# Optimization experiments

Hardware: AMD Instinct MI355X
Metric: run time of the kernel (lower is better)

Reference implementation:

```python
import jax, jax.numpy as jnp
import numpy as np

B, T, D, H = 2, 2048, 2048, 16
DH = D // H

def setup_inputs() -> dict:
    key = jax.random.key(0)
    k1, k2, k3 = jax.random.split(key, 3)
    x = jax.random.normal(k1, (B, T, D), dtype=jnp.float32)
    w_qkv = jax.random.normal(k2, (D, 3 * D), dtype=jnp.float32) * (1.0 / np.sqrt(D))
    w_o = jax.random.normal(k3, (D, D), dtype=jnp.float32) * (1.0 / np.sqrt(D))
    return {"x": x, "w_qkv": w_qkv, "w_o": w_o}

def reference(x, w_qkv, w_o):
    b, t, d = x.shape
    qkv = (x @ w_qkv).reshape(b, t, 3, H, DH)
    q, k, v = qkv[:, :, 0], qkv[:, :, 1], qkv[:, :, 2]  # [b,t,h,dh]
    scale = 1.0 / np.sqrt(DH).astype(np.float32)
    # scores: [b,h,t,t]
    scores = jnp.einsum('bqhd,bkhd->bhqk', q, k) * scale
    causal = jnp.tril(jnp.ones((t, t), dtype=bool))
    scores = jnp.where(causal[None, None], scores, -jnp.inf)
    attn = jax.nn.softmax(scores, axis=-1)
    out = jnp.einsum('bhqk,bkhd->bqhd', attn, v).reshape(b, t, d)
    return out @ w_o
```

## Files before the change

### kernel.cpp

```cpp
#include <hip/hip_runtime.h>
#include <hip/hip_bf16.h>

#define B_   2
#define T_   2048
#define D_   2048
#define H_   16
#define DH_  128
#define TD3_ 6144

typedef __attribute__((ext_vector_type(8))) short   short8;
typedef __attribute__((ext_vector_type(8))) unsigned short ushort8v;
typedef __attribute__((ext_vector_type(4))) float   f32x4;
typedef __attribute__((ext_vector_type(4))) float   f4v;
typedef __attribute__((ext_vector_type(4))) unsigned short u16x4;

static __device__ __forceinline__ unsigned short f2bf(float f) {
  unsigned int u = __builtin_bit_cast(unsigned int, f);
  u += 0x7FFFu + ((u >> 16) & 1u);
  return (unsigned short)(u >> 16);
}
static __device__ __forceinline__ float bf2f(unsigned short u) {
  return __builtin_bit_cast(float, (unsigned int)u << 16);
}

static __device__ __forceinline__ void gload_lds16(const unsigned short* g, unsigned short* l) {
  __builtin_amdgcn_global_load_lds((const __attribute__((address_space(1))) void*)g,
                                   (__attribute__((address_space(3))) void*)l, 16, 0, 0);
}

__global__ __launch_bounds__(256) void convert_f32_bf16(const float* __restrict__ X,
                                                        unsigned short* __restrict__ Y, int n4) {
  for (int i = blockIdx.x * blockDim.x + threadIdx.x; i < n4; i += gridDim.x * blockDim.x) {
    f4v v = ((const f4v*)X)[i];
    u16x4 o;
    o[0] = f2bf(v[0]); o[1] = f2bf(v[1]); o[2] = f2bf(v[2]); o[3] = f2bf(v[3]);
    ((u16x4*)Y)[i] = o;
  }
}

__global__ __launch_bounds__(256) void transpose_f32_bf16(const float* __restrict__ W,
                                                          unsigned short* __restrict__ WT,
                                                          int K, int N) {
  __shared__ float tile[32][33];
  int n0 = blockIdx.x * 32, k0 = blockIdx.y * 32;
  int tx = threadIdx.x & 31, ty = threadIdx.x >> 5;
#pragma unroll
  for (int r = 0; r < 4; r++)
    tile[ty + 8 * r][tx] = W[(size_t)(k0 + ty + 8 * r) * N + n0 + tx];
  __syncthreads();
#pragma unroll
  for (int r = 0; r < 4; r++)
    WT[(size_t)(n0 + ty + 8 * r) * K + k0 + tx] = f2bf(tile[tx][ty + 8 * r]);
}

__global__ __launch_bounds__(256) void vtr_kernel(const unsigned short* __restrict__ qkv,
                                                  unsigned short* __restrict__ vtg) {
  __shared__ unsigned short tile[64][68];
  const int t0 = blockIdx.x * 64;
  const int h = blockIdx.y >> 1, dh0 = (blockIdx.y & 1) * 64;
  const int b = blockIdx.z;
  const int tid = threadIdx.x;
  const unsigned short* src = qkv + (size_t)b * T_ * TD3_ + 2 * D_ + h * DH_ + dh0;
  {
    const int r = tid >> 3, cc = (tid & 7) * 8;
#pragma unroll
    for (int k = 0; k < 2; k++) {
      ushort8v v = *(const ushort8v*)(src + (size_t)(t0 + k * 32 + r) * TD3_ + cc);
      *(ushort8v*)&tile[k * 32 + r][cc] = v;
    }
  }
  __syncthreads();
  unsigned short* dst = vtg + ((size_t)(b * H_ + h) * DH_ + dh0) * T_ + t0;
  {
    const int d = tid >> 3, tc = (tid & 7) * 8;
#pragma unroll
    for (int k = 0; k < 2; k++) {
      ushort8v v;
#pragma unroll
      for (int j = 0; j < 8; j++) v[j] = tile[tc + j][k * 32 + d];
      *(ushort8v*)(dst + (size_t)(k * 32 + d) * T_ + tc) = v;
    }
  }
}

__global__ __launch_bounds__(512, 1) void gemm256(const unsigned short* __restrict__ A,
                                                  const unsigned short* __restrict__ BT,
                                                  unsigned short* __restrict__ C,
                                                  int M, int N, int K) {
  __shared__ unsigned short lA[2][2][128 * 64];
  __shared__ unsigned short lB[2][2][128 * 64];

  const int tid = threadIdx.x;
  const int bid = (int)blockIdx.x;
  const int nbx = N >> 8;
  const int npx = nbx >> 3;
  const int xcd = bid & 7, idx = bid >> 3;
  const int n0 = (xcd * npx + idx % npx) * 256;
  const int m0 = (idx / npx) * 256;
  const int l = tid & 63, lr = l & 15, lg = l >> 4;
  const int wid = tid >> 6, wm = wid >> 2, wn = wid & 3;
  const int bh = wn >> 1, br0 = (wn & 1) * 64;
  const int nk = K >> 6;

  f32x4 acc[8][4] = {};

  auto stageA = [&](int buf, int h, int kt) {
#pragma unroll
    for (int q = 0; q < 2; q++) {
      const int n = q * 512 + tid;
      const int row = n >> 3, ch = n & 7;
      gload_lds16(A + (size_t)(m0 + h * 128 + row) * K + kt * 64 + ((ch ^ (row & 7)) << 3),
                  &lA[buf][h][n * 8]);
    }
  };
  auto stageB = [&](int buf, int h, int kt) {
#pragma unroll
    for (int q = 0; q < 2; q++) {
      const int n = q * 512 + tid;
      const int row = n >> 3, ch = n & 7;
      gload_lds16(BT + (size_t)(n0 + h * 128 + row) * K + kt * 64 + ((ch ^ (row & 7)) << 3),
                  &lB[buf][h][n * 8]);
    }
  };

  stageB(0, 0, 0); stageA(0, 0, 0); stageB(0, 1, 0); stageA(0, 1, 0);
  if (nk > 1) {
    stageB(1, 0, 1); stageA(1, 0, 1);
    asm volatile("s_waitcnt vmcnt(4)" ::: "memory");
  } else {
    asm volatile("s_waitcnt vmcnt(0)" ::: "memory");
  }
  __builtin_amdgcn_s_barrier();

  short8 a[4][2], b0[2][2], b1[2][2];
  for (int kt = 0; kt < nk; kt++) {
    const int buf = kt & 1;

#pragma unroll
    for (int mi = 0; mi < 4; mi++)
#pragma unroll
      for (int kk = 0; kk < 2; kk++) {
        const int row = mi * 16 + lr;
        a[mi][kk] = *(const short8*)&lA[buf][wm][row * 64 + (((kk * 4 + lg) ^ (lr & 7)) << 3)];
      }
#pragma unroll
    for (int ni = 0; ni < 2; ni++)
#pragma unroll
      for (int kk = 0; kk < 2; kk++) {
        const int row = br0 + ni * 16 + lr;
        b0[ni][kk] = *(const short8*)&lB[buf][bh][row * 64 + (((kk * 4 + lg) ^ (lr & 7)) << 3)];
      }
    if (kt + 1 < nk) stageB(buf ^ 1, 1, kt + 1);
    __builtin_amdgcn_s_barrier();
    __builtin_amdgcn_s_setprio(1);
#pragma unroll
    for (int mi = 0; mi < 4; mi++)
#pragma unroll
      for (int ni = 0; ni < 2; ni++)
#pragma unroll
        for (int kk = 0; kk < 2; kk++)
          acc[mi][ni] = __builtin_amdgcn_mfma_f32_16x16x32_bf16(a[mi][kk], b0[ni][kk], acc[mi][ni], 0, 0, 0);
    __builtin_amdgcn_s_setprio(0);
    __builtin_amdgcn_s_barrier();

#pragma unroll
    for (int ni = 0; ni < 2; ni++)
#pragma unroll
      for (int kk = 0; kk < 2; kk++) {
        const int row = br0 + (2 + ni) * 16 + lr;
        b1[ni][kk] = *(const short8*)&lB[buf][bh][row * 64 + (((kk * 4 + lg) ^ (lr & 7)) << 3)];
      }
    if (kt + 1 < nk) stageA(buf ^ 1, 1, kt + 1);
    __builtin_amdgcn_s_barrier();
    __builtin_amdgcn_s_setprio(1);
#pragma unroll
    for (int mi = 0; mi < 4; mi++)
#pragma unroll
      for (int ni = 0; ni < 2; ni++)
#pragma unroll
        for (int kk = 0; kk < 2; kk++)
          acc[mi][2 + ni] = __builtin_amdgcn_mfma_f32_16x16x32_bf16(a[mi][kk], b1[ni][kk], acc[mi][2 + ni], 0, 0, 0);
    __builtin_amdgcn_s_setprio(0);
    __builtin_amdgcn_s_barrier();

#pragma unroll
    for (int mi = 0; mi < 4; mi++)
#pragma unroll
      for (int kk = 0; kk < 2; kk++) {
        const int row = (4 + mi) * 16 + lr;
        a[mi][kk] = *(const short8*)&lA[buf][wm][row * 64 + (((kk * 4 + lg) ^ (lr & 7)) << 3)];
      }
    if (kt + 2 < nk) stageB(buf, 0, kt + 2);
    __builtin_amdgcn_s_barrier();
    __builtin_amdgcn_s_setprio(1);
#pragma unroll
    for (int mi = 0; mi < 4; mi++)
#pragma unroll
      for (int ni = 0; ni < 2; ni++)
#pragma unroll
        for (int kk = 0; kk < 2; kk++)
          acc[4 + mi][2 + ni] = __builtin_amdgcn_mfma_f32_16x16x32_bf16(a[mi][kk], b1[ni][kk], acc[4 + mi][2 + ni], 0, 0, 0);
    __builtin_amdgcn_s_setprio(0);
    __builtin_amdgcn_s_barrier();

    if (kt + 2 < nk) stageA(buf, 0, kt + 2);
    __builtin_amdgcn_s_barrier();
    __builtin_amdgcn_s_setprio(1);
#pragma unroll
    for (int mi = 0; mi < 4; mi++)
#pragma unroll
      for (int ni = 0; ni < 2; ni++)
#pragma unroll
        for (int kk = 0; kk < 2; kk++)
          acc[4 + mi][ni] = __builtin_amdgcn_mfma_f32_16x16x32_bf16(a[mi][kk], b0[ni][kk], acc[4 + mi][ni], 0, 0, 0);
    __builtin_amdgcn_s_setprio(0);
    if (kt + 2 < nk) asm volatile("s_waitcnt vmcnt(4)" ::: "memory");
    else             asm volatile("s_waitcnt vmcnt(0)" ::: "memory");
    __builtin_amdgcn_s_barrier();
  }

#pragma unroll
  for (int mi = 0; mi < 8; mi++)
#pragma unroll
    for (int ni = 0; ni < 4; ni++)
#pragma unroll
      for (int i = 0; i < 4; i++) {
        const int row = m0 + wm * 128 + mi * 16 + lg * 4 + i;
        const int col = n0 + wn * 64 + ni * 16 + lr;
        C[(size_t)row * N + col] = f2bf(acc[mi][ni][i]);
      }
}

__global__ __launch_bounds__(512, 1) void gemm_op(const unsigned short* __restrict__ A,
                                                  const unsigned short* __restrict__ BT,
                                                  float* __restrict__ C,
                                                  int M, int N, int K) {
  __shared__ unsigned short lA[2][128 * 64];
  __shared__ unsigned short lB[2][2][128 * 64];

  const int tid = threadIdx.x;
  const int bid = (int)blockIdx.x;
  const int xcd = bid & 7, idx = bid >> 3;
  const int n0 = xcd * 256, m0 = idx * 128;
  const int l = tid & 63, lr = l & 15, lg = l >> 4;
  const int wid = tid >> 6, wm = wid >> 2, wn = wid & 3;
  const int bh = wn >> 1, br0 = (wn & 1) * 64;
  const int nk = K >> 6;

  f32x4 acc[4][4] = {};

  auto stageA = [&](int buf, int kt) {
#pragma unroll
    for (int q = 0; q < 2; q++) {
      const int n = q * 512 + tid;
      const int row = n >> 3, ch = n & 7;
      gload_lds16(A + (size_t)(m0 + row) * K + kt * 64 + ((ch ^ (row & 7)) << 3),
                  &lA[buf][n * 8]);
    }
  };
  auto stageB = [&](int buf, int h, int kt) {
#pragma unroll
    for (int q = 0; q < 2; q++) {
      const int n = q * 512 + tid;
      const int row = n >> 3, ch = n & 7;
      gload_lds16(BT + (size_t)(n0 + h * 128 + row) * K + kt * 64 + ((ch ^ (row & 7)) << 3),
                  &lB[buf][h][n * 8]);
    }
  };

  stageB(0, 0, 0); stageB(0, 1, 0); stageA(0, 0);
  asm volatile("s_waitcnt vmcnt(0)" ::: "memory");
  __builtin_amdgcn_s_barrier();

  short8 a[4][2], b0[2][2], b1[2][2];
  for (int kt = 0; kt < nk; kt++) {
    const int buf = kt & 1;

    if (kt + 1 < nk) { stageB(buf ^ 1, 0, kt + 1); stageB(buf ^ 1, 1, kt + 1); stageA(buf ^ 1, kt + 1); }
#pragma unroll
    for (int mi = 0; mi < 4; mi++)
#pragma unroll
      for (int kk = 0; kk < 2; kk++) {
        const int row = wm * 64 + mi * 16 + lr;
        a[mi][kk] = *(const short8*)&lA[buf][row * 64 + (((kk * 4 + lg) ^ (lr & 7)) << 3)];
      }
#pragma unroll
    for (int ni = 0; ni < 2; ni++)
#pragma unroll
      for (int kk = 0; kk < 2; kk++) {
        const int row = br0 + ni * 16 + lr;
        b0[ni][kk] = *(const short8*)&lB[buf][bh][row * 64 + (((kk * 4 + lg) ^ (lr & 7)) << 3)];
      }
    __builtin_amdgcn_s_barrier();
    __builtin_amdgcn_s_setprio(1);
#pragma unroll
    for (int mi = 0; mi < 4; mi++)
#pragma unroll
      for (int ni = 0; ni < 2; ni++)
#pragma unroll
        for (int kk = 0; kk < 2; kk++)
          acc[mi][ni] = __builtin_amdgcn_mfma_f32_16x16x32_bf16(a[mi][kk], b0[ni][kk], acc[mi][ni], 0, 0, 0);
    __builtin_amdgcn_s_setprio(0);
    __builtin_amdgcn_s_barrier();

#pragma unroll
    for (int ni = 0; ni < 2; ni++)
#pragma unroll
      for (int kk = 0; kk < 2; kk++) {
        const int row = br0 + (2 + ni) * 16 + lr;
        b1[ni][kk] = *(const short8*)&lB[buf][bh][row * 64 + (((kk * 4 + lg) ^ (lr & 7)) << 3)];
      }
    __builtin_amdgcn_s_barrier();
    __builtin_amdgcn_s_setprio(1);
#pragma unroll
    for (int mi = 0; mi < 4; mi++)
#pragma unroll
      for (int ni = 0; ni < 2; ni++)
#pragma unroll
        for (int kk = 0; kk < 2; kk++)
          acc[mi][2 + ni] = __builtin_amdgcn_mfma_f32_16x16x32_bf16(a[mi][kk], b1[ni][kk], acc[mi][2 + ni], 0, 0, 0);
    __builtin_amdgcn_s_setprio(0);
    asm volatile("s_waitcnt vmcnt(0)" ::: "memory");
    __builtin_amdgcn_s_barrier();
  }

#pragma unroll
  for (int mi = 0; mi < 4; mi++)
#pragma unroll
    for (int ni = 0; ni < 4; ni++)
#pragma unroll
      for (int i = 0; i < 4; i++) {
        const int row = m0 + wm * 64 + mi * 16 + lg * 4 + i;
        const int col = n0 + wn * 64 + ni * 16 + lr;
        C[(size_t)row * N + col] = acc[mi][ni][i];
      }
}

__global__ __launch_bounds__(256, 2) void attn_fa(const unsigned short* __restrict__ qkv,
                                                  const unsigned short* __restrict__ vtg,
                                                  unsigned short* __restrict__ out) {
  const int x = blockIdx.x, h = blockIdx.y, b = blockIdx.z;
  const int qtl = b ? x : (T_ / 128 - 1 - x);
  const int q0 = qtl * 128;
  const int tid = threadIdx.x, w = tid >> 6, l = tid & 63, lr = l & 15, lg = l >> 4;

  const unsigned short* Qb = qkv + (size_t)b * T_ * TD3_ + h * DH_;
  const unsigned short* Kb = Qb + D_;
  const unsigned short* Vt = vtg + ((size_t)b * H_ + h) * DH_ * T_;

  __shared__ unsigned short klds[2][64 * 128];
  __shared__ unsigned short vt[2][128 * 64];
  __shared__ unsigned short plds[4][32 * 64];

  const float scale = 0.08838834764831845f;

  short8 qf[2][4];
#pragma unroll
  for (int mi = 0; mi < 2; mi++) {
    const unsigned short* qrow = Qb + (size_t)(q0 + w * 32 + mi * 16 + lr) * TD3_;
#pragma unroll
    for (int ks = 0; ks < 4; ks++) {
      ushort8v qv = *(const ushort8v*)(qrow + ks * 32 + lg * 8);
      short8 qs;
#pragma unroll
      for (int j = 0; j < 8; j++) qs[j] = (short)f2bf(bf2f(qv[j]) * scale);
      qf[mi][ks] = qs;
    }
  }

  f32x4 oacc[2][8] = {};
  float mrun[2][4], lsum[2][4];
#pragma unroll
  for (int mi = 0; mi < 2; mi++)
#pragma unroll
    for (int i = 0; i < 4; i++) { mrun[mi][i] = -__builtin_inff(); lsum[mi][i] = 0.f; }

  auto STAGE = [&](int buf, int kv0) {
#pragma unroll
    for (int it = 0; it < 4; it++) {
      const int n = it * 256 + tid;
      { const int kv = n >> 4, ch = n & 15;
        gload_lds16(Kb + (size_t)(kv0 + kv) * TD3_ + ((ch ^ (kv & 7)) << 3),
                    &klds[buf][n * 8]); }
      { const int dh = n >> 3, ch = n & 7;
        gload_lds16(Vt + (size_t)dh * T_ + kv0 + ((ch ^ (dh & 7)) << 3),
                    &vt[buf][n * 8]); }
    }
  };

  const int nt = 2 * qtl + 2;
  STAGE(0, 0);
  __syncthreads();

  for (int t = 0; t < nt; t++) {
    const int buf = t & 1;
    if (t + 1 < nt) STAGE(buf ^ 1, (t + 1) * 64);

    const int kv0 = t * 64;
    const bool active = (kv0 <= q0 + w * 32 + 31);
    if (active) {
      f32x4 s[2][4] = {};
      __builtin_amdgcn_s_setprio(1);
#pragma unroll
      for (int nf = 0; nf < 4; nf++) {
        const int kv = nf * 16 + lr;
#pragma unroll
        for (int ks = 0; ks < 4; ks++) {
          short8 kf = *(const short8*)&klds[buf][kv * 128 + (((ks * 4 + lg) ^ (lr & 7)) << 3)];
#pragma unroll
          for (int mi = 0; mi < 2; mi++)
            s[mi][nf] = __builtin_amdgcn_mfma_f32_16x16x32_bf16(qf[mi][ks], kf, s[mi][nf], 0, 0, 0);
        }
      }
      __builtin_amdgcn_s_setprio(0);

      const bool needmask = (kv0 + 63 > q0 + w * 32);
      float pmax[2][4];
#pragma unroll
      for (int mi = 0; mi < 2; mi++)
#pragma unroll
        for (int i = 0; i < 4; i++) pmax[mi][i] = -__builtin_inff();
#pragma unroll
      for (int mi = 0; mi < 2; mi++)
#pragma unroll
        for (int nf = 0; nf < 4; nf++)
#pragma unroll
          for (int i = 0; i < 4; i++) {
            float xv = s[mi][nf][i];
            if (needmask) {
              const int qr = w * 32 + mi * 16 + lg * 4 + i;
              const int kc = nf * 16 + lr;
              if (kv0 + kc > q0 + qr) xv = -__builtin_inff();
            }
            s[mi][nf][i] = xv;
            pmax[mi][i] = fmaxf(pmax[mi][i], xv);
          }
#pragma unroll
      for (int m = 1; m < 16; m <<= 1)
#pragma unroll
        for (int mi = 0; mi < 2; mi++)
#pragma unroll
          for (int i = 0; i < 4; i++) pmax[mi][i] = fmaxf(pmax[mi][i], __shfl_xor(pmax[mi][i], m));

      float alpha[2][4], rsum[2][4];
#pragma unroll
      for (int mi = 0; mi < 2; mi++)
#pragma unroll
        for (int i = 0; i < 4; i++) {
          const float mn = fmaxf(mrun[mi][i], pmax[mi][i]);
          alpha[mi][i] = __expf(mrun[mi][i] - mn);
          mrun[mi][i] = mn;
          rsum[mi][i] = 0.f;
        }
#pragma unroll
      for (int mi = 0; mi < 2; mi++)
#pragma unroll
        for (int nf = 0; nf < 4; nf++)
#pragma unroll
          for (int i = 0; i < 4; i++) {
            const float p = __expf(s[mi][nf][i] - mrun[mi][i]);
            rsum[mi][i] += p;
            const int prow = mi * 16 + lg * 4 + i;
            plds[w][prow * 64 + ((nf * 16 + lr) ^ ((prow & 7) << 3))] = f2bf(p);
          }
#pragma unroll
      for (int m = 1; m < 16; m <<= 1)
#pragma unroll
        for (int mi = 0; mi < 2; mi++)
#pragma unroll
          for (int i = 0; i < 4; i++) rsum[mi][i] += __shfl_xor(rsum[mi][i], m);
#pragma unroll
      for (int mi = 0; mi < 2; mi++)
#pragma unroll
        for (int i = 0; i < 4; i++) lsum[mi][i] = lsum[mi][i] * alpha[mi][i] + rsum[mi][i];
#pragma unroll
      for (int mi = 0; mi < 2; mi++)
#pragma unroll
        for (int nf = 0; nf < 8; nf++)
#pragma unroll
          for (int i = 0; i < 4; i++) oacc[mi][nf][i] *= alpha[mi][i];

      __builtin_amdgcn_s_setprio(1);
#pragma unroll
      for (int kk = 0; kk < 2; kk++) {
        short8 pa[2];
#pragma unroll
        for (int mi = 0; mi < 2; mi++) {
          const int prow = mi * 16 + lr;
          pa[mi] = *(const short8*)&plds[w][prow * 64 + (((kk * 32 + lg * 8)) ^ ((prow & 7) << 3))];
        }
#pragma unroll
        for (int nf = 0; nf < 8; nf++) {
          const short8 vb = *(const short8*)&vt[buf][(nf * 16 + lr) * 64 + (((kk * 4 + lg) ^ (lr & 7)) << 3)];
#pragma unroll
          for (int mi = 0; mi < 2; mi++)
            oacc[mi][nf] = __builtin_amdgcn_mfma_f32_16x16x32_bf16(pa[mi], vb, oacc[mi][nf], 0, 0, 0);
        }
      }
      __builtin_amdgcn_s_setprio(0);
    }
    __syncthreads();
  }

  float rinv[2][4];
#pragma unroll
  for (int mi = 0; mi < 2; mi++)
#pragma unroll
    for (int i = 0; i < 4; i++) rinv[mi][i] = 1.f / lsum[mi][i];
#pragma unroll
  for (int mi = 0; mi < 2; mi++) {
    unsigned short* orow = out + ((size_t)b * T_ + q0 + w * 32 + mi * 16 + lg * 4) * D_ + h * DH_;
#pragma unroll
    for (int nf = 0; nf < 8; nf++)
#pragma unroll
      for (int i = 0; i < 4; i++)
        orow[(size_t)i * D_ + nf * 16 + lr] = f2bf(oacc[mi][nf][i] * rinv[mi][i]);
  }
}

extern "C" void kernel_launch(void* const* d_in, const int* in_sizes, int n_in,
                              void* d_out, int out_size, void* d_ws, size_t ws_size,
                              hipStream_t stream) {
  const float* x    = (const float*)d_in[0];
  const float* wqkv = (const float*)d_in[1];
  const float* wo   = (const float*)d_in[2];
  float* out = (float*)d_out;

  char* ws = (char*)d_ws;
  unsigned short* xb    = (unsigned short*)(ws);
  unsigned short* wqkvt = (unsigned short*)(ws + 16777216);
  unsigned short* vtg   = (unsigned short*)(ws + 16777216);
  unsigned short* wot   = (unsigned short*)(ws + 41943040);
  unsigned short* qkv   = (unsigned short*)(ws + 50331648);
  unsigned short* attn  = xb;

  convert_f32_bf16<<<2048, 256, 0, stream>>>(x, xb, B_ * T_ * D_ / 4);
  transpose_f32_bf16<<<dim3(TD3_ / 32, D_ / 32), 256, 0, stream>>>(wqkv, wqkvt, D_, TD3_);
  transpose_f32_bf16<<<dim3(D_ / 32, D_ / 32), 256, 0, stream>>>(wo, wot, D_, D_);

  gemm256<<<dim3((TD3_ / 256) * ((B_ * T_) / 256)), 512, 0, stream>>>(xb, wqkvt, qkv,
                                                                      B_ * T_, TD3_, D_);
  vtr_kernel<<<dim3(T_ / 64, H_ * 2, B_), 256, 0, stream>>>(qkv, vtg);
  attn_fa<<<dim3(T_ / 128, H_, B_), 256, 0, stream>>>(qkv, vtg, attn);
  gemm_op<<<dim3((D_ / 256) * ((B_ * T_) / 128)), 512, 0, stream>>>(attn, wot, out,
                                                                    B_ * T_, D_, D_);
}
```

Baseline: 307.4 us.

## Retile QKV GEMM to 256x192 blocks and deepen out-projection GEMM pipeline

The QKV projection GEMM moves from 256x256 to 256x192 output tiles, giving 512 workgroups instead of 384 so the grid fills the 256 CUs in exact waves. Each wave now owns 48 columns and the B loads are restaged in thirds. The output-projection GEMM gains a two-stage prefetch with partial vmcnt waits and splits its MFMA work into four phases, so global loads overlap compute instead of draining every iteration. The smaller tile reuses loaded data less, and the waitcnt bookkeeping is fragile if the load counts are wrong.

```diff
diff --git a/kernel.cpp b/kernel.cpp
--- a/kernel.cpp
+++ b/kernel.cpp
@@ -83,26 +83,24 @@
   }
 }
 
-__global__ __launch_bounds__(512, 1) void gemm256(const unsigned short* __restrict__ A,
-                                                  const unsigned short* __restrict__ BT,
-                                                  unsigned short* __restrict__ C,
-                                                  int M, int N, int K) {
+__global__ __launch_bounds__(512, 1) void gemm_qkv192(const unsigned short* __restrict__ A,
+                                                      const unsigned short* __restrict__ BT,
+                                                      unsigned short* __restrict__ C,
+                                                      int M, int N, int K) {
   __shared__ unsigned short lA[2][2][128 * 64];
-  __shared__ unsigned short lB[2][2][128 * 64];
+  __shared__ unsigned short lB[2][192 * 64];
 
   const int tid = threadIdx.x;
   const int bid = (int)blockIdx.x;
-  const int nbx = N >> 8;
-  const int npx = nbx >> 3;
+  const int npx = 4;
   const int xcd = bid & 7, idx = bid >> 3;
-  const int n0 = (xcd * npx + idx % npx) * 256;
-  const int m0 = (idx / npx) * 256;
+  const int n0 = (xcd * npx + (idx & 3)) * 192;
+  const int m0 = (idx >> 2) * 256;
   const int l = tid & 63, lr = l & 15, lg = l >> 4;
   const int wid = tid >> 6, wm = wid >> 2, wn = wid & 3;
-  const int bh = wn >> 1, br0 = (wn & 1) * 64;
   const int nk = K >> 6;
 
-  f32x4 acc[8][4] = {};
+  f32x4 acc[8][3] = {};
 
   auto stageA = [&](int buf, int h, int kt) {
 #pragma unroll
@@ -113,26 +111,23 @@
                   &lA[buf][h][n * 8]);
     }
   };
-  auto stageB = [&](int buf, int h, int kt) {
-#pragma unroll
-    for (int q = 0; q < 2; q++) {
-      const int n = q * 512 + tid;
-      const int row = n >> 3, ch = n & 7;
-      gload_lds16(BT + (size_t)(n0 + h * 128 + row) * K + kt * 64 + ((ch ^ (row & 7)) << 3),
-                  &lB[buf][h][n * 8]);
-    }
+  auto stageBt = [&](int buf, int third, int kt) {
+    const int r = tid >> 3, ch = tid & 7;
+    gload_lds16(BT + (size_t)(n0 + third * 64 + r) * K + kt * 64 + ((ch ^ (r & 7)) << 3),
+                &lB[buf][third * 4096 + tid * 8]);
   };
 
-  stageB(0, 0, 0); stageA(0, 0, 0); stageB(0, 1, 0); stageA(0, 1, 0);
+  stageA(0, 0, 0); stageA(0, 1, 0);
+  stageBt(0, 0, 0); stageBt(0, 1, 0); stageBt(0, 2, 0);
   if (nk > 1) {
-    stageB(1, 0, 1); stageA(1, 0, 1);
-    asm volatile("s_waitcnt vmcnt(4)" ::: "memory");
+    stageBt(1, 0, 1); stageBt(1, 1, 1); stageBt(1, 2, 1);
+    asm volatile("s_waitcnt vmcnt(3)" ::: "memory");
   } else {
     asm volatile("s_waitcnt vmcnt(0)" ::: "memory");
   }
   __builtin_amdgcn_s_barrier();
 
-  short8 a[4][2], b0[2][2], b1[2][2];
+  short8 a[4][2], b[3][2];
   for (int kt = 0; kt < nk; kt++) {
     const int buf = kt & 1;
 
@@ -144,13 +139,13 @@
         a[mi][kk] = *(const short8*)&lA[buf][wm][row * 64 + (((kk * 4 + lg) ^ (lr & 7)) << 3)];
       }
 #pragma unroll
-    for (int ni = 0; ni < 2; ni++)
-#pragma unroll
-      for (int kk = 0; kk < 2; kk++) {
-        const int row = br0 + ni * 16 + lr;
-        b0[ni][kk] = *(const short8*)&lB[buf][bh][row * 64 + (((kk * 4 + lg) ^ (lr & 7)) << 3)];
-      }
-    if (kt + 1 < nk) stageB(buf ^ 1, 1, kt + 1);
+    for (int ni = 0; ni < 3; ni++)
+#pragma unroll
+      for (int kk = 0; kk < 2; kk++) {
+        const int row = wn * 48 + ni * 16 + lr;
+        b[ni][kk] = *(const short8*)&lB[buf][row * 64 + (((kk * 4 + lg) ^ (lr & 7)) << 3)];
+      }
+    if (kt + 1 < nk) stageA(buf ^ 1, 0, kt + 1);
     __builtin_amdgcn_s_barrier();
     __builtin_amdgcn_s_setprio(1);
 #pragma unroll
@@ -159,27 +154,19 @@
       for (int ni = 0; ni < 2; ni++)
 #pragma unroll
         for (int kk = 0; kk < 2; kk++)
-          acc[mi][ni] = __builtin_amdgcn_mfma_f32_16x16x32_bf16(a[mi][kk], b0[ni][kk], acc[mi][ni], 0, 0, 0);
-    __builtin_amdgcn_s_setprio(0);
-    __builtin_amdgcn_s_barrier();
-
-#pragma unroll
-    for (int ni = 0; ni < 2; ni++)
-#pragma unroll
-      for (int kk = 0; kk < 2; kk++) {
-        const int row = br0 + (2 + ni) * 16 + lr;
-        b1[ni][kk] = *(const short8*)&lB[buf][bh][row * 64 + (((kk * 4 + lg) ^ (lr & 7)) << 3)];
-      }
+          acc[mi][ni] = __builtin_amdgcn_mfma_f32_16x16x32_bf16(a[mi][kk], b[ni][kk], acc[mi][ni], 0, 0, 0);
+    __builtin_amdgcn_s_setprio(0);
+    __builtin_amdgcn_s_barrier();
+
     if (kt + 1 < nk) stageA(buf ^ 1, 1, kt + 1);
+    if (kt + 2 < nk) stageBt(buf, 0, kt + 2);
     __builtin_amdgcn_s_barrier();
     __builtin_amdgcn_s_setprio(1);
 #pragma unroll
     for (int mi = 0; mi < 4; mi++)
 #pragma unroll
-      for (int ni = 0; ni < 2; ni++)
-#pragma unroll
-        for (int kk = 0; kk < 2; kk++)
-          acc[mi][2 + ni] = __builtin_amdgcn_mfma_f32_16x16x32_bf16(a[mi][kk], b1[ni][kk], acc[mi][2 + ni], 0, 0, 0);
+      for (int kk = 0; kk < 2; kk++)
+        acc[mi][2] = __builtin_amdgcn_mfma_f32_16x16x32_bf16(a[mi][kk], b[2][kk], acc[mi][2], 0, 0, 0);
     __builtin_amdgcn_s_setprio(0);
     __builtin_amdgcn_s_barrier();
 
@@ -190,7 +177,7 @@
         const int row = (4 + mi) * 16 + lr;
         a[mi][kk] = *(const short8*)&lA[buf][wm][row * 64 + (((kk * 4 + lg) ^ (lr & 7)) << 3)];
       }
-    if (kt + 2 < nk) stageB(buf, 0, kt + 2);
+    if (kt + 2 < nk) stageBt(buf, 1, kt + 2);
     __builtin_amdgcn_s_barrier();
     __builtin_amdgcn_s_setprio(1);
 #pragma unroll
@@ -199,22 +186,20 @@
       for (int ni = 0; ni < 2; ni++)
 #pragma unroll
         for (int kk = 0; kk < 2; kk++)
-          acc[4 + mi][2 + ni] = __builtin_amdgcn_mfma_f32_16x16x32_bf16(a[mi][kk], b1[ni][kk], acc[4 + mi][2 + ni], 0, 0, 0);
-    __builtin_amdgcn_s_setprio(0);
-    __builtin_amdgcn_s_barrier();
-
-    if (kt + 2 < nk) stageA(buf, 0, kt + 2);
+          acc[4 + mi][ni] = __builtin_amdgcn_mfma_f32_16x16x32_bf16(a[mi][kk], b[ni][kk], acc[4 + mi][ni], 0, 0, 0);
+    __builtin_amdgcn_s_setprio(0);
+    __builtin_amdgcn_s_barrier();
+
+    if (kt + 2 < nk) stageBt(buf, 2, kt + 2);
     __builtin_amdgcn_s_barrier();
     __builtin_amdgcn_s_setprio(1);
 #pragma unroll
     for (int mi = 0; mi < 4; mi++)
 #pragma unroll
-      for (int ni = 0; ni < 2; ni++)
-#pragma unroll
-        for (int kk = 0; kk < 2; kk++)
-          acc[4 + mi][ni] = __builtin_amdgcn_mfma_f32_16x16x32_bf16(a[mi][kk], b0[ni][kk], acc[4 + mi][ni], 0, 0, 0);
-    __builtin_amdgcn_s_setprio(0);
-    if (kt + 2 < nk) asm volatile("s_waitcnt vmcnt(4)" ::: "memory");
+      for (int kk = 0; kk < 2; kk++)
+        acc[4 + mi][2] = __builtin_amdgcn_mfma_f32_16x16x32_bf16(a[mi][kk], b[2][kk], acc[4 + mi][2], 0, 0, 0);
+    __builtin_amdgcn_s_setprio(0);
+    if (kt + 2 < nk) asm volatile("s_waitcnt vmcnt(3)" ::: "memory");
     else             asm volatile("s_waitcnt vmcnt(0)" ::: "memory");
     __builtin_amdgcn_s_barrier();
   }
@@ -222,19 +207,19 @@
 #pragma unroll
   for (int mi = 0; mi < 8; mi++)
 #pragma unroll
-    for (int ni = 0; ni < 4; ni++)
+    for (int ni = 0; ni < 3; ni++)
 #pragma unroll
       for (int i = 0; i < 4; i++) {
         const int row = m0 + wm * 128 + mi * 16 + lg * 4 + i;
-        const int col = n0 + wn * 64 + ni * 16 + lr;
+        const int col = n0 + wn * 48 + ni * 16 + lr;
         C[(size_t)row * N + col] = f2bf(acc[mi][ni][i]);
       }
 }
 
-__global__ __launch_bounds__(512, 1) void gemm_op(const unsigned short* __restrict__ A,
-                                                  const unsigned short* __restrict__ BT,
-                                                  float* __restrict__ C,
-                                                  int M, int N, int K) {
+__global__ __launch_bounds__(512, 1) void gemm_op8(const unsigned short* __restrict__ A,
+                                                   const unsigned short* __restrict__ BT,
+                                                   float* __restrict__ C,
+                                                   int M, int N, int K) {
   __shared__ unsigned short lA[2][128 * 64];
   __shared__ unsigned short lB[2][2][128 * 64];
 
@@ -269,16 +254,20 @@
   };
 
   stageB(0, 0, 0); stageB(0, 1, 0); stageA(0, 0);
-  asm volatile("s_waitcnt vmcnt(0)" ::: "memory");
+  if (nk > 1) {
+    stageB(1, 0, 1); stageB(1, 1, 1); stageA(1, 1);
+    asm volatile("s_waitcnt vmcnt(6)" ::: "memory");
+  } else {
+    asm volatile("s_waitcnt vmcnt(0)" ::: "memory");
+  }
   __builtin_amdgcn_s_barrier();
 
-  short8 a[4][2], b0[2][2], b1[2][2];
+  short8 a[2][2], b0[2][2], b1[2][2];
   for (int kt = 0; kt < nk; kt++) {
     const int buf = kt & 1;
 
-    if (kt + 1 < nk) { stageB(buf ^ 1, 0, kt + 1); stageB(buf ^ 1, 1, kt + 1); stageA(buf ^ 1, kt + 1); }
-#pragma unroll
-    for (int mi = 0; mi < 4; mi++)
+#pragma unroll
+    for (int mi = 0; mi < 2; mi++)
 #pragma unroll
       for (int kk = 0; kk < 2; kk++) {
         const int row = wm * 64 + mi * 16 + lr;
@@ -294,7 +283,7 @@
     __builtin_amdgcn_s_barrier();
     __builtin_amdgcn_s_setprio(1);
 #pragma unroll
-    for (int mi = 0; mi < 4; mi++)
+    for (int mi = 0; mi < 2; mi++)
 #pragma unroll
       for (int ni = 0; ni < 2; ni++)
 #pragma unroll
@@ -313,14 +302,48 @@
     __builtin_amdgcn_s_barrier();
     __builtin_amdgcn_s_setprio(1);
 #pragma unroll
-    for (int mi = 0; mi < 4; mi++)
+    for (int mi = 0; mi < 2; mi++)
 #pragma unroll
       for (int ni = 0; ni < 2; ni++)
 #pragma unroll
         for (int kk = 0; kk < 2; kk++)
           acc[mi][2 + ni] = __builtin_amdgcn_mfma_f32_16x16x32_bf16(a[mi][kk], b1[ni][kk], acc[mi][2 + ni], 0, 0, 0);
     __builtin_amdgcn_s_setprio(0);
-    asm volatile("s_waitcnt vmcnt(0)" ::: "memory");
+    __builtin_amdgcn_s_barrier();
+
+#pragma unroll
+    for (int mi = 0; mi < 2; mi++)
+#pragma unroll
+      for (int kk = 0; kk < 2; kk++) {
+        const int row = wm * 64 + (2 + mi) * 16 + lr;
+        a[mi][kk] = *(const short8*)&lA[buf][row * 64 + (((kk * 4 + lg) ^ (lr & 7)) << 3)];
+      }
+    if (kt + 2 < nk) stageB(buf, 0, kt + 2);
+    __builtin_amdgcn_s_barrier();
+    __builtin_amdgcn_s_setprio(1);
+#pragma unroll
+    for (int mi = 0; mi < 2; mi++)
+#pragma unroll
+      for (int ni = 0; ni < 2; ni++)
+#pragma unroll
+        for (int kk = 0; kk < 2; kk++)
+          acc[2 + mi][2 + ni] = __builtin_amdgcn_mfma_f32_16x16x32_bf16(a[mi][kk], b1[ni][kk], acc[2 + mi][2 + ni], 0, 0, 0);
+    __builtin_amdgcn_s_setprio(0);
+    __builtin_amdgcn_s_barrier();
+
+    if (kt + 2 < nk) { stageB(buf, 1, kt + 2); stageA(buf, kt + 2); }
+    __builtin_amdgcn_s_barrier();
+    __builtin_amdgcn_s_setprio(1);
+#pragma unroll
+    for (int mi = 0; mi < 2; mi++)
+#pragma unroll
+      for (int ni = 0; ni < 2; ni++)
+#pragma unroll
+        for (int kk = 0; kk < 2; kk++)
+          acc[2 + mi][ni] = __builtin_amdgcn_mfma_f32_16x16x32_bf16(a[mi][kk], b0[ni][kk], acc[2 + mi][ni], 0, 0, 0);
+    __builtin_amdgcn_s_setprio(0);
+    if (kt + 2 < nk) asm volatile("s_waitcnt vmcnt(6)" ::: "memory");
+    else             asm volatile("s_waitcnt vmcnt(0)" ::: "memory");
     __builtin_amdgcn_s_barrier();
   }
 
@@ -538,10 +561,8 @@
   transpose_f32_bf16<<<dim3(TD3_ / 32, D_ / 32), 256, 0, stream>>>(wqkv, wqkvt, D_, TD3_);
   transpose_f32_bf16<<<dim3(D_ / 32, D_ / 32), 256, 0, stream>>>(wo, wot, D_, D_);
 
-  gemm256<<<dim3((TD3_ / 256) * ((B_ * T_) / 256)), 512, 0, stream>>>(xb, wqkvt, qkv,
-                                                                      B_ * T_, TD3_, D_);
+  gemm_qkv192<<<dim3(512), 512, 0, stream>>>(xb, wqkvt, qkv, B_ * T_, TD3_, D_);
   vtr_kernel<<<dim3(T_ / 64, H_ * 2, B_), 256, 0, stream>>>(qkv, vtg);
   attn_fa<<<dim3(T_ / 128, H_, B_), 256, 0, stream>>>(qkv, vtg, attn);
-  gemm_op<<<dim3((D_ / 256) * ((B_ * T_) / 128)), 512, 0, stream>>>(attn, wot, out,
-                                                                    B_ * T_, D_, D_);
-}
+  gemm_op8<<<dim3(256), 512, 0, stream>>>(attn, wot, out, B_ * T_, D_, D_);
+}
```

New measurement: 302.4 us. No clear change (-1.6%).
